# Kernel tuning notes

Measured on AMD Instinct MI355X. Metric: run time of the kernel, lower is better.

## Reference

```python
import jax, jax.numpy as jnp
import numpy as np


def setup_inputs() -> dict:
    key = jax.random.key(0)
    k1, k2, k3 = jax.random.split(key, 3)
    B, Sq, Sk, H, Hk, D = 2, 2048, 2048, 16, 4, 64
    q = jax.random.normal(k1, (B, Sq, H, D), dtype=jnp.float32)
    kv = jax.random.normal(k2, (B, Sk, 2, Hk, D), dtype=jnp.float32)
    key_padding_mask = jax.random.randint(k3, (B, Sk), 0, 2).astype(bool)
    return {"q": q, "kv": kv, "key_padding_mask": key_padding_mask}


def reference(q, kv, key_padding_mask):
    # q: (B, Sq, H, D); kv: (B, Sk, 2, Hk, D); key_padding_mask: (B, Sk) bool (True = keep)
    B, Sq, H, D = q.shape
    Hk = kv.shape[3]
    if Hk != H:
        # GQA: repeat kv heads so (... hkv d) -> (... (hkv g) d)
        kv = jnp.repeat(kv, H // Hk, axis=3)
    k = kv[:, :, 0]  # (B, Sk, H, D)
    v = kv[:, :, 1]  # (B, Sk, H, D)
    softmax_scale = 1.0 / jnp.sqrt(jnp.asarray(D, dtype=q.dtype))
    scores = jnp.einsum('bthd,bshd->bhts', q, k * softmax_scale)  # (B, H, Sq, Sk)
    # additive padding mask: 0 where keep, -10000 where masked (matches torch code)
    pad = jnp.where(key_padding_mask, jnp.asarray(0.0, scores.dtype),
                    jnp.asarray(-10000.0, scores.dtype))
    scores = scores + pad[:, None, None, :]
    attention = jax.nn.softmax(scores, axis=-1)
    # dropout rate is 0.0 -> identity
    output = jnp.einsum('bhts,bshd->bthd', attention, v)  # (B, Sq, H, D)
    return output
```

## Files before the change

kernel.cpp:

```cpp
#include <hip/hip_runtime.h>
#include <hip/hip_bf16.h>
#include <stdint.h>

typedef __bf16 bf16_t;
typedef bf16_t bf16x8 __attribute__((ext_vector_type(8)));
typedef bf16_t bf16x4 __attribute__((ext_vector_type(4)));
typedef float f32x4 __attribute__((ext_vector_type(4)));
typedef float f32x16 __attribute__((ext_vector_type(16)));
typedef uint32_t u32x4 __attribute__((ext_vector_type(4)));
typedef int   i32x4 __attribute__((ext_vector_type(4)));

#define BB 2
#define SQ 2048
#define SK 2048
#define NH 16
#define HKV 4
#define DD 64
#define GQ 4
#define MTILE 128
#define NTILE 64
#define MAXNT 32

#define KTILE_BYTES 8192
#define CNT_OFF   ((size_t)0)
#define CIDX_OFF  ((size_t)1024)
#define PADC_OFF  (CIDX_OFF + (size_t)BB * SK * 4)
#define KC_OFF    ((size_t)65536)
#define VC_OFF    (KC_OFF + (size_t)BB * HKV * MAXNT * KTILE_BYTES)

__device__ __forceinline__ int swzK(int row, int colByte) {
    return row * 128 + (colByte ^ ((row & 7) << 4));
}

#define GLDS(g, l) __builtin_amdgcn_global_load_lds( \
    (const __attribute__((address_space(1))) void*)(g), \
    (__attribute__((address_space(3))) void*)(l), 16, 0, 0)

__global__ __launch_bounds__(256)
void scan_kernel(const int* __restrict__ mask, char* __restrict__ ws)
{
    __shared__ int wtot[4];
    const int b    = blockIdx.x;
    const int tid  = threadIdx.x;
    const int lane = tid & 63;
    const int wid  = tid >> 6;

    int m[8], c = 0;
    {
        const int base = b * SK + tid * 8;
        i32x4 a0 = *(const i32x4*)&mask[base];
        i32x4 a1 = *(const i32x4*)&mask[base + 4];
        #pragma unroll
        for (int j = 0; j < 4; ++j) { m[j] = a0[j] ? 1 : 0; c += m[j]; }
        #pragma unroll
        for (int j = 0; j < 4; ++j) { m[4 + j] = a1[j] ? 1 : 0; c += m[4 + j]; }
    }
    int sc = c;
    #pragma unroll
    for (int off = 1; off < 64; off <<= 1) {
        int n = __shfl_up(sc, off, 64);
        if (lane >= off) sc += n;
    }
    if (lane == 63) wtot[wid] = sc;
    __syncthreads();
    int wbase = 0;
    #pragma unroll
    for (int w = 0; w < 4; ++w) if (w < wid) wbase += wtot[w];
    const int total = wtot[0] + wtot[1] + wtot[2] + wtot[3];

    int* cidx = (int*)(ws + CIDX_OFF) + b * SK;
    int pos = wbase + sc - c;
    #pragma unroll
    for (int j = 0; j < 8; ++j)
        if (m[j]) cidx[pos++] = tid * 8 + j;

    if (tid == 0) ((int*)(ws + CNT_OFF))[b] = total;

    float* padc = (float*)(ws + PADC_OFF) + b * SK;
    for (int i = tid; i < SK; i += 256)
        padc[i] = (i < total) ? 0.f : -30000.f;
}

__global__ __launch_bounds__(256)
void gather_kernel(const float* __restrict__ kv, char* __restrict__ ws)
{
    const int bid  = blockIdx.x;
    const int tile = bid & 31;
    const int bh   = bid >> 5;
    const int hk   = bh & 3;
    const int b    = bh >> 2;

    const int cnt = ((const int*)(ws + CNT_OFF))[b];
    const int nt  = (cnt + 63) >> 6;
    if (tile >= nt) return;

    const int tid = threadIdx.x;
    const int s4  = tid >> 4;
    const int d0  = (tid & 15) * 4;

    const int* cidx = (const int*)(ws + CIDX_OFF) + b * SK;
    bf16_t* Kt = (bf16_t*)(ws + KC_OFF + (size_t)bid * KTILE_BYTES);
    bf16_t* Vt = (bf16_t*)(ws + VC_OFF + (size_t)bid * KTILE_BYTES);

    f32x4 kk4[4], vv4[4];
    #pragma unroll
    for (int p = 0; p < 4; ++p) {
        const int crow = tile * NTILE + s4 * 4 + p;
        if (crow < cnt) {
            const int s = cidx[crow];
            const float* base = kv + (size_t)((b * SK + s) * 2) * (HKV * DD) + hk * DD + d0;
            kk4[p] = *(const f32x4*)base;
            vv4[p] = *(const f32x4*)(base + HKV * DD);
        } else {
            kk4[p] = (f32x4)(0.f);
            vv4[p] = (f32x4)(0.f);
        }
    }
    #pragma unroll
    for (int p = 0; p < 4; ++p) {
        bf16x4 kb;
        #pragma unroll
        for (int j = 0; j < 4; ++j) kb[j] = (bf16_t)kk4[p][j];
        *(bf16x4*)((char*)Kt + swzK(s4 * 4 + p, d0 * 2)) = kb;
    }
    #pragma unroll
    for (int j = 0; j < 4; ++j) {
        bf16x4 tv;
        #pragma unroll
        for (int p = 0; p < 4; ++p) tv[p] = (bf16_t)vv4[p][j];
        *(bf16x4*)((char*)Vt + swzK(d0 + j, s4 * 8)) = tv;
    }
}

__global__ __launch_bounds__(256, 2)
void fattn32p(const float* __restrict__ q, const char* __restrict__ ws,
              float* __restrict__ out)
{
    __shared__ __align__(16) bf16_t Ks[4][NTILE * 64];
    __shared__ __align__(16) bf16_t Vs[4][DD * 64];

    const int tid  = threadIdx.x;
    const int wid  = tid >> 6;
    const int lane = tid & 63;
    const int l31  = lane & 31;
    const int hf   = lane >> 5;
    const int ef   = lane & 7;

    const int bid = (blockIdx.x & 7) * 64 + (blockIdx.x >> 3);
    const int qt  = bid & 15;
    const int bh  = bid >> 4;
    const int hq  = bh & 15;
    const int b   = bh >> 4;
    const int hk  = hq / GQ;

    const int cnt = ((const int*)(ws + CNT_OFF))[b];
    const int nt  = (cnt + 63) >> 6;

    const int qrow0 = qt * MTILE + wid * 32;
    const float SC = 0.18033688011112042f;

    bf16x8 qf[4];
    {
        const float* qp = q + ((size_t)(b * SQ + qrow0 + l31) * NH + hq) * DD;
        #pragma unroll
        for (int kblk = 0; kblk < 4; ++kblk) {
            f32x4 v0 = *(const f32x4*)(qp + kblk * 16 + hf * 8);
            f32x4 v1 = *(const f32x4*)(qp + kblk * 16 + hf * 8 + 4);
            #pragma unroll
            for (int j = 0; j < 4; ++j) {
                qf[kblk][j]     = (bf16_t)(v0[j] * SC);
                qf[kblk][4 + j] = (bf16_t)(v1[j] * SC);
            }
        }
    }

    const char* kgb = ws + KC_OFF + (size_t)((b * HKV + hk) * MAXNT) * KTILE_BYTES;
    const char* vgb = ws + VC_OFF + (size_t)((b * HKV + hk) * MAXNT) * KTILE_BYTES;
    const float* padcb = (const float*)(ws + PADC_OFF) + b * SK;

    auto STAGE = [&](int t, int buf) {
        const char* ksrc = kgb + (size_t)t * KTILE_BYTES + wid * 2048 + lane * 16;
        const char* vsrc = vgb + (size_t)t * KTILE_BYTES + wid * 2048 + lane * 16;
        char* kdst = (char*)Ks[buf] + wid * 2048;
        char* vdst = (char*)Vs[buf] + wid * 2048;
        GLDS(ksrc, kdst);
        GLDS(ksrc + 1024, kdst + 1024);
        GLDS(vsrc, vdst);
        GLDS(vsrc + 1024, vdst + 1024);
    };

    int colX[4];
    #pragma unroll
    for (int kblk = 0; kblk < 4; ++kblk)
        colX[kblk] = (kblk * 32 + hf * 16) ^ (ef << 4);

    f32x16 o0, o1;
    #pragma unroll
    for (int i = 0; i < 16; ++i) { o0[i] = 0.f; o1[i] = 0.f; }
    float l_run = 0.f;

    auto QK = [&](int t, int buf, f32x16& s0, f32x16& s1) {
        if (t == nt - 1) {
            #pragma unroll
            for (int a = 0; a < 4; ++a) {
                f32x4 p0 = *(const f32x4*)(padcb + t * 64 + a * 8 + hf * 4);
                f32x4 p1 = *(const f32x4*)(padcb + t * 64 + 32 + a * 8 + hf * 4);
                #pragma unroll
                for (int c = 0; c < 4; ++c) { s0[a * 4 + c] = p0[c]; s1[a * 4 + c] = p1[c]; }
            }
        } else {
            #pragma unroll
            for (int i = 0; i < 16; ++i) { s0[i] = 0.f; s1[i] = 0.f; }
        }
        __builtin_amdgcn_s_setprio(1);
        #pragma unroll
        for (int kblk = 0; kblk < 4; ++kblk) {
            bf16x8 kf0 = *(const bf16x8*)((char*)Ks[buf] + l31 * 128 + colX[kblk]);
            bf16x8 kf1 = *(const bf16x8*)((char*)Ks[buf] + 4096 + l31 * 128 + colX[kblk]);
            s0 = __builtin_amdgcn_mfma_f32_32x32x16_bf16(kf0, qf[kblk], s0, 0, 0, 0);
            s1 = __builtin_amdgcn_mfma_f32_32x32x16_bf16(kf1, qf[kblk], s1, 0, 0, 0);
        }
        __builtin_amdgcn_s_setprio(0);
    };

    auto SM = [&](f32x16& s0, f32x16& s1, bf16x8* paw) {
        #pragma unroll
        for (int i = 0; i < 16; ++i) {
            s0[i] = __builtin_amdgcn_exp2f(s0[i]);
            s1[i] = __builtin_amdgcn_exp2f(s1[i]);
        }
        float t0 = 0.f, t1 = 0.f, t2 = 0.f, t3 = 0.f;
        #pragma unroll
        for (int i = 0; i < 4; ++i) {
            t0 += s0[i]      + s1[i];
            t1 += s0[4 + i]  + s1[4 + i];
            t2 += s0[8 + i]  + s1[8 + i];
            t3 += s0[12 + i] + s1[12 + i];
        }
        l_run += (t0 + t1) + (t2 + t3);

        #pragma unroll
        for (int ks2 = 0; ks2 < 4; ++ks2) {
            const int aX = (ks2 & 1) * 2;
            uint32_t X0, X1, Y0, Y1;
            #define CVTPK(dst, lo, hi) asm("v_cvt_pk_bf16_f32 %0, %1, %2" : "=v"(dst) : "v"(lo), "v"(hi))
            if (ks2 & 2) {
                CVTPK(X0, s1[4*aX + 0], s1[4*aX + 1]);
                CVTPK(X1, s1[4*aX + 2], s1[4*aX + 3]);
                CVTPK(Y0, s1[4*aX + 4], s1[4*aX + 5]);
                CVTPK(Y1, s1[4*aX + 6], s1[4*aX + 7]);
            } else {
                CVTPK(X0, s0[4*aX + 0], s0[4*aX + 1]);
                CVTPK(X1, s0[4*aX + 2], s0[4*aX + 3]);
                CVTPK(Y0, s0[4*aX + 4], s0[4*aX + 5]);
                CVTPK(Y1, s0[4*aX + 6], s0[4*aX + 7]);
            }
            #undef CVTPK
            asm("v_permlane32_swap_b32 %0, %1" : "+v"(X0), "+v"(Y0));
            asm("v_permlane32_swap_b32 %0, %1" : "+v"(X1), "+v"(Y1));
            union { u32x4 w; bf16x8 v; } u;
            u.w[0] = X0; u.w[1] = X1; u.w[2] = Y0; u.w[3] = Y1;
            paw[ks2] = u.v;
        }
    };

    auto PV = [&](int buf, const bf16x8* paw) {
        __builtin_amdgcn_s_setprio(1);
        #pragma unroll
        for (int ks2 = 0; ks2 < 4; ++ks2) {
            bf16x8 vf0 = *(const bf16x8*)((char*)Vs[buf] + l31 * 128 + colX[ks2]);
            bf16x8 vf1 = *(const bf16x8*)((char*)Vs[buf] + 4096 + l31 * 128 + colX[ks2]);
            o0 = __builtin_amdgcn_mfma_f32_32x32x16_bf16(paw[ks2], vf0, o0, 0, 0, 0);
            o1 = __builtin_amdgcn_mfma_f32_32x32x16_bf16(paw[ks2], vf1, o1, 0, 0, 0);
        }
        __builtin_amdgcn_s_setprio(0);
    };

    STAGE(0, 0);
    if (1 < nt) STAGE(1, 1);

    int t = 0;
    for (; t + 1 < nt; t += 2) {
        const int n2 = (t + 2 < nt) ? 1 : 0;
        const int n3 = (t + 3 < nt) ? 1 : 0;
        if (n2) STAGE(t + 2, (t + 2) & 3);
        if (n3) STAGE(t + 3, (t + 3) & 3);
        if (n2 + n3 == 2)      asm volatile("s_waitcnt vmcnt(8)" ::: "memory");
        else if (n2 + n3 == 1) asm volatile("s_waitcnt vmcnt(4)" ::: "memory");
        else                   asm volatile("s_waitcnt vmcnt(0)" ::: "memory");
        __builtin_amdgcn_s_barrier();
        __builtin_amdgcn_sched_barrier(0);

        f32x16 sA0, sA1, sB0, sB1;
        bf16x8 pawA[4], pawB[4];
        QK(t,     t & 3,       sA0, sA1);
        QK(t + 1, (t + 1) & 3, sB0, sB1);
        SM(sA0, sA1, pawA);
        PV(t & 3, pawA);
        SM(sB0, sB1, pawB);
        PV((t + 1) & 3, pawB);

        __builtin_amdgcn_sched_barrier(0);
        __builtin_amdgcn_s_barrier();
    }
    if (t < nt) {
        asm volatile("s_waitcnt vmcnt(0)" ::: "memory");
        __builtin_amdgcn_s_barrier();
        __builtin_amdgcn_sched_barrier(0);
        f32x16 sA0, sA1;
        bf16x8 pawA[4];
        QK(t, t & 3, sA0, sA1);
        SM(sA0, sA1, pawA);
        PV(t & 3, pawA);
    }

    float lt = l_run + __shfl_xor(l_run, 32, 64);
    #pragma unroll
    for (int r = 0; r < 16; ++r) {
        const int t_r = (r & 3) + 8 * (r >> 2) + 4 * hf;
        const float den = __shfl(lt, t_r, 64);
        const float linv = den > 0.f ? 1.f / den : 0.f;
        float* op = out + ((size_t)(b * SQ + qrow0 + t_r) * NH + hq) * DD + l31;
        op[0]  = o0[r] * linv;
        op[32] = o1[r] * linv;
    }
}

extern "C" void kernel_launch(void* const* d_in, const int* in_sizes, int n_in,
                              void* d_out, int out_size, void* d_ws, size_t ws_size,
                              hipStream_t stream) {
    const float* q    = (const float*)d_in[0];
    const float* kv   = (const float*)d_in[1];
    const int*   mask = (const int*)d_in[2];
    float* out = (float*)d_out;

    scan_kernel<<<BB, 256, 0, stream>>>(mask, (char*)d_ws);
    gather_kernel<<<BB * HKV * MAXNT, 256, 0, stream>>>(kv, (char*)d_ws);
    fattn32p<<<BB * NH * (SQ / MTILE), 256, 0, stream>>>(q, (const char*)d_ws, out);
}
```

Measured before the change: 42.02 us.

## Split KV range across two blocks, fuse scan into gather, add combine pass

Fuses the mask prefix scan into the gather kernel, with each block recomputing the scan and keeping only its 64-entry window in shared memory. The attention kernel is split in two along the key dimension, doubling the grid, cutting LDS to two buffers and raising occupancy to 4 blocks per CU. Unnormalized partial outputs and row sums go to workspace, and a new combine kernel merges and normalizes them. The padding mask is now computed inline instead of loaded, and the LDS swizzle changes to 8-byte granularity with split 64-bit loads. The trade-off is an extra kernel launch plus extra global writes and reads of two full fp32 partial outputs.

```diff
diff --git a/kernel.cpp b/kernel.cpp
--- a/kernel.cpp
+++ b/kernel.cpp
@@ -20,16 +20,19 @@
 #define MTILE 128
 #define NTILE 64
 #define MAXNT 32
+#define NSPLIT 2
 
 #define KTILE_BYTES 8192
 #define CNT_OFF   ((size_t)0)
-#define CIDX_OFF  ((size_t)1024)
-#define PADC_OFF  (CIDX_OFF + (size_t)BB * SK * 4)
-#define KC_OFF    ((size_t)65536)
+#define KC_OFF    ((size_t)4096)
 #define VC_OFF    (KC_OFF + (size_t)BB * HKV * MAXNT * KTILE_BYTES)
-
-__device__ __forceinline__ int swzK(int row, int colByte) {
-    return row * 128 + (colByte ^ ((row & 7) << 4));
+#define OP_OFF    (VC_OFF + (size_t)BB * HKV * MAXNT * KTILE_BYTES)
+#define OP_SPLIT  ((size_t)BB * SQ * NH * DD)
+#define LP_OFF    (OP_OFF + (size_t)NSPLIT * OP_SPLIT * 4)
+#define LP_SPLIT  ((size_t)BB * SQ * NH)
+
+__device__ __forceinline__ int swz8(int row, int colByte) {
+    return row * 128 + (colByte ^ ((row & 15) << 3));
 }
 
 #define GLDS(g, l) __builtin_amdgcn_global_load_lds( \
@@ -37,10 +40,17 @@
     (__attribute__((address_space(3))) void*)(l), 16, 0, 0)
 
 __global__ __launch_bounds__(256)
-void scan_kernel(const int* __restrict__ mask, char* __restrict__ ws)
+void gather_kernel(const float* __restrict__ kv, const int* __restrict__ mask,
+                   char* __restrict__ ws)
 {
     __shared__ int wtot[4];
-    const int b    = blockIdx.x;
+    __shared__ int cwin[NTILE];
+
+    const int bid  = blockIdx.x;
+    const int tile = bid & 31;
+    const int bh   = bid >> 5;
+    const int hk   = bh & 3;
+    const int b    = bh >> 2;
     const int tid  = threadIdx.x;
     const int lane = tid & 63;
     const int wid  = tid >> 6;
@@ -66,48 +76,36 @@
     int wbase = 0;
     #pragma unroll
     for (int w = 0; w < 4; ++w) if (w < wid) wbase += wtot[w];
-    const int total = wtot[0] + wtot[1] + wtot[2] + wtot[3];
-
-    int* cidx = (int*)(ws + CIDX_OFF) + b * SK;
+    const int cnt = wtot[0] + wtot[1] + wtot[2] + wtot[3];
+
+    if (hk == 0 && tile == 0 && tid == 0)
+        ((int*)(ws + CNT_OFF))[b] = cnt;
+
+    const int w0 = tile * NTILE;
     int pos = wbase + sc - c;
     #pragma unroll
     for (int j = 0; j < 8; ++j)
-        if (m[j]) cidx[pos++] = tid * 8 + j;
-
-    if (tid == 0) ((int*)(ws + CNT_OFF))[b] = total;
-
-    float* padc = (float*)(ws + PADC_OFF) + b * SK;
-    for (int i = tid; i < SK; i += 256)
-        padc[i] = (i < total) ? 0.f : -30000.f;
-}
-
-__global__ __launch_bounds__(256)
-void gather_kernel(const float* __restrict__ kv, char* __restrict__ ws)
-{
-    const int bid  = blockIdx.x;
-    const int tile = bid & 31;
-    const int bh   = bid >> 5;
-    const int hk   = bh & 3;
-    const int b    = bh >> 2;
-
-    const int cnt = ((const int*)(ws + CNT_OFF))[b];
-    const int nt  = (cnt + 63) >> 6;
+        if (m[j]) {
+            if (pos >= w0 && pos < w0 + NTILE) cwin[pos - w0] = tid * 8 + j;
+            ++pos;
+        }
+    __syncthreads();
+
+    const int nt = (cnt + 63) >> 6;
     if (tile >= nt) return;
 
-    const int tid = threadIdx.x;
-    const int s4  = tid >> 4;
-    const int d0  = (tid & 15) * 4;
-
-    const int* cidx = (const int*)(ws + CIDX_OFF) + b * SK;
+    const int s4 = tid >> 4;
+    const int d0 = (tid & 15) * 4;
+
     bf16_t* Kt = (bf16_t*)(ws + KC_OFF + (size_t)bid * KTILE_BYTES);
     bf16_t* Vt = (bf16_t*)(ws + VC_OFF + (size_t)bid * KTILE_BYTES);
 
     f32x4 kk4[4], vv4[4];
     #pragma unroll
     for (int p = 0; p < 4; ++p) {
-        const int crow = tile * NTILE + s4 * 4 + p;
+        const int crow = w0 + s4 * 4 + p;
         if (crow < cnt) {
-            const int s = cidx[crow];
+            const int s = cwin[s4 * 4 + p];
             const float* base = kv + (size_t)((b * SK + s) * 2) * (HKV * DD) + hk * DD + d0;
             kk4[p] = *(const f32x4*)base;
             vv4[p] = *(const f32x4*)(base + HKV * DD);
@@ -121,32 +119,32 @@
         bf16x4 kb;
         #pragma unroll
         for (int j = 0; j < 4; ++j) kb[j] = (bf16_t)kk4[p][j];
-        *(bf16x4*)((char*)Kt + swzK(s4 * 4 + p, d0 * 2)) = kb;
+        *(bf16x4*)((char*)Kt + swz8(s4 * 4 + p, d0 * 2)) = kb;
     }
     #pragma unroll
     for (int j = 0; j < 4; ++j) {
         bf16x4 tv;
         #pragma unroll
         for (int p = 0; p < 4; ++p) tv[p] = (bf16_t)vv4[p][j];
-        *(bf16x4*)((char*)Vt + swzK(d0 + j, s4 * 8)) = tv;
-    }
-}
-
-__global__ __launch_bounds__(256, 2)
-void fattn32p(const float* __restrict__ q, const char* __restrict__ ws,
-              float* __restrict__ out)
+        *(bf16x4*)((char*)Vt + swz8(d0 + j, s4 * 8)) = tv;
+    }
+}
+
+__global__ __launch_bounds__(256, 4)
+void fattn_split(const float* __restrict__ q, char* __restrict__ ws)
 {
-    __shared__ __align__(16) bf16_t Ks[4][NTILE * 64];
-    __shared__ __align__(16) bf16_t Vs[4][DD * 64];
+    __shared__ __align__(16) bf16_t Ks[2][NTILE * 64];
+    __shared__ __align__(16) bf16_t Vs[2][DD * 64];
 
     const int tid  = threadIdx.x;
     const int wid  = tid >> 6;
     const int lane = tid & 63;
     const int l31  = lane & 31;
     const int hf   = lane >> 5;
-    const int ef   = lane & 7;
-
-    const int bid = (blockIdx.x & 7) * 64 + (blockIdx.x >> 3);
+
+    const int bidx = (blockIdx.x & 7) * 128 + (blockIdx.x >> 3);
+    const int sp  = bidx & 1;
+    const int bid = bidx >> 1;
     const int qt  = bid & 15;
     const int bh  = bid >> 4;
     const int hq  = bh & 15;
@@ -155,6 +153,9 @@
 
     const int cnt = ((const int*)(ws + CNT_OFF))[b];
     const int nt  = (cnt + 63) >> 6;
+    const int nth = (nt + 1) >> 1;
+    const int tbeg = sp ? nth : 0;
+    const int tend = sp ? nt : nth;
 
     const int qrow0 = qt * MTILE + wid * 32;
     const float SC = 0.18033688011112042f;
@@ -176,7 +177,6 @@
 
     const char* kgb = ws + KC_OFF + (size_t)((b * HKV + hk) * MAXNT) * KTILE_BYTES;
     const char* vgb = ws + VC_OFF + (size_t)((b * HKV + hk) * MAXNT) * KTILE_BYTES;
-    const float* padcb = (const float*)(ws + PADC_OFF) + b * SK;
 
     auto STAGE = [&](int t, int buf) {
         const char* ksrc = kgb + (size_t)t * KTILE_BYTES + wid * 2048 + lane * 16;
@@ -189,41 +189,56 @@
         GLDS(vsrc + 1024, vdst + 1024);
     };
 
-    int colX[4];
-    #pragma unroll
-    for (int kblk = 0; kblk < 4; ++kblk)
-        colX[kblk] = (kblk * 32 + hf * 16) ^ (ef << 4);
+    auto LD8 = [&](const bf16_t* T, int row, int cB) -> bf16x8 {
+        const char* p = (const char*)T + row * 128;
+        const int x = (row & 15) << 3;
+        union { bf16x4 h[2]; bf16x8 v; } u;
+        u.h[0] = *(const bf16x4*)(p + (cB ^ x));
+        u.h[1] = *(const bf16x4*)(p + ((cB + 8) ^ x));
+        return u.v;
+    };
 
     f32x16 o0, o1;
     #pragma unroll
     for (int i = 0; i < 16; ++i) { o0[i] = 0.f; o1[i] = 0.f; }
     float l_run = 0.f;
 
-    auto QK = [&](int t, int buf, f32x16& s0, f32x16& s1) {
+    if (tbeg < tend) STAGE(tbeg, 0);
+
+    for (int t = tbeg; t < tend; ++t) {
+        const int cur = (t - tbeg) & 1;
+        if (t + 1 < tend) {
+            STAGE(t + 1, cur ^ 1);
+            asm volatile("s_waitcnt vmcnt(4)" ::: "memory");
+        } else {
+            asm volatile("s_waitcnt vmcnt(0)" ::: "memory");
+        }
+        __builtin_amdgcn_s_barrier();
+        __builtin_amdgcn_sched_barrier(0);
+
+        f32x16 s0, s1;
         if (t == nt - 1) {
             #pragma unroll
-            for (int a = 0; a < 4; ++a) {
-                f32x4 p0 = *(const f32x4*)(padcb + t * 64 + a * 8 + hf * 4);
-                f32x4 p1 = *(const f32x4*)(padcb + t * 64 + 32 + a * 8 + hf * 4);
-                #pragma unroll
-                for (int c = 0; c < 4; ++c) { s0[a * 4 + c] = p0[c]; s1[a * 4 + c] = p1[c]; }
+            for (int i = 0; i < 16; ++i) {
+                const int sl = (i & 3) + 8 * (i >> 2) + 4 * hf;
+                s0[i] = (t * 64 + sl      < cnt) ? 0.f : -30000.f;
+                s1[i] = (t * 64 + sl + 32 < cnt) ? 0.f : -30000.f;
             }
         } else {
             #pragma unroll
             for (int i = 0; i < 16; ++i) { s0[i] = 0.f; s1[i] = 0.f; }
         }
+
         __builtin_amdgcn_s_setprio(1);
         #pragma unroll
         for (int kblk = 0; kblk < 4; ++kblk) {
-            bf16x8 kf0 = *(const bf16x8*)((char*)Ks[buf] + l31 * 128 + colX[kblk]);
-            bf16x8 kf1 = *(const bf16x8*)((char*)Ks[buf] + 4096 + l31 * 128 + colX[kblk]);
+            bf16x8 kf0 = LD8(Ks[cur], l31,      kblk * 32 + hf * 16);
+            bf16x8 kf1 = LD8(Ks[cur], 32 + l31, kblk * 32 + hf * 16);
             s0 = __builtin_amdgcn_mfma_f32_32x32x16_bf16(kf0, qf[kblk], s0, 0, 0, 0);
             s1 = __builtin_amdgcn_mfma_f32_32x32x16_bf16(kf1, qf[kblk], s1, 0, 0, 0);
         }
         __builtin_amdgcn_s_setprio(0);
-    };
-
-    auto SM = [&](f32x16& s0, f32x16& s1, bf16x8* paw) {
+
         #pragma unroll
         for (int i = 0; i < 16; ++i) {
             s0[i] = __builtin_amdgcn_exp2f(s0[i]);
@@ -239,6 +254,7 @@
         }
         l_run += (t0 + t1) + (t2 + t3);
 
+        bf16x8 paw[4];
         #pragma unroll
         for (int ks2 = 0; ks2 < 4; ++ks2) {
             const int aX = (ks2 & 1) * 2;
@@ -262,68 +278,56 @@
             u.w[0] = X0; u.w[1] = X1; u.w[2] = Y0; u.w[3] = Y1;
             paw[ks2] = u.v;
         }
-    };
-
-    auto PV = [&](int buf, const bf16x8* paw) {
+
         __builtin_amdgcn_s_setprio(1);
         #pragma unroll
         for (int ks2 = 0; ks2 < 4; ++ks2) {
-            bf16x8 vf0 = *(const bf16x8*)((char*)Vs[buf] + l31 * 128 + colX[ks2]);
-            bf16x8 vf1 = *(const bf16x8*)((char*)Vs[buf] + 4096 + l31 * 128 + colX[ks2]);
+            bf16x8 vf0 = LD8(Vs[cur], l31,      ks2 * 32 + hf * 16);
+            bf16x8 vf1 = LD8(Vs[cur], 32 + l31, ks2 * 32 + hf * 16);
             o0 = __builtin_amdgcn_mfma_f32_32x32x16_bf16(paw[ks2], vf0, o0, 0, 0, 0);
             o1 = __builtin_amdgcn_mfma_f32_32x32x16_bf16(paw[ks2], vf1, o1, 0, 0, 0);
         }
         __builtin_amdgcn_s_setprio(0);
-    };
-
-    STAGE(0, 0);
-    if (1 < nt) STAGE(1, 1);
-
-    int t = 0;
-    for (; t + 1 < nt; t += 2) {
-        const int n2 = (t + 2 < nt) ? 1 : 0;
-        const int n3 = (t + 3 < nt) ? 1 : 0;
-        if (n2) STAGE(t + 2, (t + 2) & 3);
-        if (n3) STAGE(t + 3, (t + 3) & 3);
-        if (n2 + n3 == 2)      asm volatile("s_waitcnt vmcnt(8)" ::: "memory");
-        else if (n2 + n3 == 1) asm volatile("s_waitcnt vmcnt(4)" ::: "memory");
-        else                   asm volatile("s_waitcnt vmcnt(0)" ::: "memory");
-        __builtin_amdgcn_s_barrier();
-        __builtin_amdgcn_sched_barrier(0);
-
-        f32x16 sA0, sA1, sB0, sB1;
-        bf16x8 pawA[4], pawB[4];
-        QK(t,     t & 3,       sA0, sA1);
-        QK(t + 1, (t + 1) & 3, sB0, sB1);
-        SM(sA0, sA1, pawA);
-        PV(t & 3, pawA);
-        SM(sB0, sB1, pawB);
-        PV((t + 1) & 3, pawB);
 
         __builtin_amdgcn_sched_barrier(0);
         __builtin_amdgcn_s_barrier();
     }
-    if (t < nt) {
-        asm volatile("s_waitcnt vmcnt(0)" ::: "memory");
-        __builtin_amdgcn_s_barrier();
-        __builtin_amdgcn_sched_barrier(0);
-        f32x16 sA0, sA1;
-        bf16x8 pawA[4];
-        QK(t, t & 3, sA0, sA1);
-        SM(sA0, sA1, pawA);
-        PV(t & 3, pawA);
-    }
 
     float lt = l_run + __shfl_xor(l_run, 32, 64);
+    float* OP = (float*)(ws + OP_OFF) + (size_t)sp * OP_SPLIT;
+    float* LP = (float*)(ws + LP_OFF) + (size_t)sp * LP_SPLIT;
     #pragma unroll
     for (int r = 0; r < 16; ++r) {
         const int t_r = (r & 3) + 8 * (r >> 2) + 4 * hf;
-        const float den = __shfl(lt, t_r, 64);
-        const float linv = den > 0.f ? 1.f / den : 0.f;
-        float* op = out + ((size_t)(b * SQ + qrow0 + t_r) * NH + hq) * DD + l31;
-        op[0]  = o0[r] * linv;
-        op[32] = o1[r] * linv;
-    }
+        const size_t R = ((size_t)(b * SQ + qrow0 + t_r) * NH + hq);
+        OP[R * 64 + l31]      = o0[r];
+        OP[R * 64 + 32 + l31] = o1[r];
+    }
+    if (hf == 0) {
+        const size_t R = ((size_t)(b * SQ + qrow0 + l31) * NH + hq);
+        LP[R] = lt;
+    }
+}
+
+__global__ __launch_bounds__(256)
+void combine_kernel(const char* __restrict__ ws, float* __restrict__ out)
+{
+    const int gid = blockIdx.x * 256 + threadIdx.x;
+    const size_t R = (size_t)(gid >> 4);
+    const int c4 = (gid & 15) * 4;
+    const float* P0 = (const float*)(ws + OP_OFF);
+    const float* P1 = P0 + OP_SPLIT;
+    const float* L0 = (const float*)(ws + LP_OFF);
+    const float* L1 = L0 + LP_SPLIT;
+
+    f32x4 a = *(const f32x4*)&P0[R * 64 + c4];
+    f32x4 c = *(const f32x4*)&P1[R * 64 + c4];
+    const float den = L0[R] + L1[R];
+    const float inv = den > 0.f ? 1.f / den : 0.f;
+    f32x4 o;
+    #pragma unroll
+    for (int j = 0; j < 4; ++j) o[j] = (a[j] + c[j]) * inv;
+    *(f32x4*)&out[R * 64 + c4] = o;
 }
 
 extern "C" void kernel_launch(void* const* d_in, const int* in_sizes, int n_in,
@@ -334,7 +338,7 @@
     const int*   mask = (const int*)d_in[2];
     float* out = (float*)d_out;
 
-    scan_kernel<<<BB, 256, 0, stream>>>(mask, (char*)d_ws);
-    gather_kernel<<<BB * HKV * MAXNT, 256, 0, stream>>>(kv, (char*)d_ws);
-    fattn32p<<<BB * NH * (SQ / MTILE), 256, 0, stream>>>(q, (const char*)d_ws, out);
-}
+    gather_kernel<<<BB * HKV * MAXNT, 256, 0, stream>>>(kv, mask, (char*)d_ws);
+    fattn_split<<<BB * NH * (SQ / MTILE) * NSPLIT, 256, 0, stream>>>(q, (char*)d_ws);
+    combine_kernel<<<(BB * SQ * NH * 16) / 256, 256, 0, stream>>>((const char*)d_ws, out);
+}
```

Result: slower. 51.11 us (+21.6%).

## Fuse mask scan into gather kernel and compute padding inline

Applied to the files above, without the earlier changes.

Merges the scan and gather kernels so each gather block redoes the prefix scan over the mask and keeps only its own 64-entry index window in shared memory, which drops one launch and the global index buffer. The padding bias is now computed in registers from the count rather than read from a workspace array. The K/V swizzle moves to an 8-byte granularity over 16 rows, so each 16-byte fragment read becomes two 8-byte LDS reads. The cost is the scan being repeated across 256 blocks and twice as many LDS read instructions in the inner loop.

```diff
diff --git a/kernel.cpp b/kernel.cpp
--- a/kernel.cpp
+++ b/kernel.cpp
@@ -23,13 +23,11 @@
 
 #define KTILE_BYTES 8192
 #define CNT_OFF   ((size_t)0)
-#define CIDX_OFF  ((size_t)1024)
-#define PADC_OFF  (CIDX_OFF + (size_t)BB * SK * 4)
-#define KC_OFF    ((size_t)65536)
+#define KC_OFF    ((size_t)4096)
 #define VC_OFF    (KC_OFF + (size_t)BB * HKV * MAXNT * KTILE_BYTES)
 
-__device__ __forceinline__ int swzK(int row, int colByte) {
-    return row * 128 + (colByte ^ ((row & 7) << 4));
+__device__ __forceinline__ int swz8(int row, int colByte) {
+    return row * 128 + (colByte ^ ((row & 15) << 3));
 }
 
 #define GLDS(g, l) __builtin_amdgcn_global_load_lds( \
@@ -37,10 +35,17 @@
     (__attribute__((address_space(3))) void*)(l), 16, 0, 0)
 
 __global__ __launch_bounds__(256)
-void scan_kernel(const int* __restrict__ mask, char* __restrict__ ws)
+void gather_kernel(const float* __restrict__ kv, const int* __restrict__ mask,
+                   char* __restrict__ ws)
 {
     __shared__ int wtot[4];
-    const int b    = blockIdx.x;
+    __shared__ int cwin[NTILE];
+
+    const int bid  = blockIdx.x;
+    const int tile = bid & 31;
+    const int bh   = bid >> 5;
+    const int hk   = bh & 3;
+    const int b    = bh >> 2;
     const int tid  = threadIdx.x;
     const int lane = tid & 63;
     const int wid  = tid >> 6;
@@ -66,48 +71,36 @@
     int wbase = 0;
     #pragma unroll
     for (int w = 0; w < 4; ++w) if (w < wid) wbase += wtot[w];
-    const int total = wtot[0] + wtot[1] + wtot[2] + wtot[3];
-
-    int* cidx = (int*)(ws + CIDX_OFF) + b * SK;
+    const int cnt = wtot[0] + wtot[1] + wtot[2] + wtot[3];
+
+    if (hk == 0 && tile == 0 && tid == 0)
+        ((int*)(ws + CNT_OFF))[b] = cnt;
+
+    const int w0 = tile * NTILE;
     int pos = wbase + sc - c;
     #pragma unroll
     for (int j = 0; j < 8; ++j)
-        if (m[j]) cidx[pos++] = tid * 8 + j;
-
-    if (tid == 0) ((int*)(ws + CNT_OFF))[b] = total;
-
-    float* padc = (float*)(ws + PADC_OFF) + b * SK;
-    for (int i = tid; i < SK; i += 256)
-        padc[i] = (i < total) ? 0.f : -30000.f;
-}
-
-__global__ __launch_bounds__(256)
-void gather_kernel(const float* __restrict__ kv, char* __restrict__ ws)
-{
-    const int bid  = blockIdx.x;
-    const int tile = bid & 31;
-    const int bh   = bid >> 5;
-    const int hk   = bh & 3;
-    const int b    = bh >> 2;
-
-    const int cnt = ((const int*)(ws + CNT_OFF))[b];
-    const int nt  = (cnt + 63) >> 6;
+        if (m[j]) {
+            if (pos >= w0 && pos < w0 + NTILE) cwin[pos - w0] = tid * 8 + j;
+            ++pos;
+        }
+    __syncthreads();
+
+    const int nt = (cnt + 63) >> 6;
     if (tile >= nt) return;
 
-    const int tid = threadIdx.x;
-    const int s4  = tid >> 4;
-    const int d0  = (tid & 15) * 4;
-
-    const int* cidx = (const int*)(ws + CIDX_OFF) + b * SK;
+    const int s4 = tid >> 4;
+    const int d0 = (tid & 15) * 4;
+
     bf16_t* Kt = (bf16_t*)(ws + KC_OFF + (size_t)bid * KTILE_BYTES);
     bf16_t* Vt = (bf16_t*)(ws + VC_OFF + (size_t)bid * KTILE_BYTES);
 
     f32x4 kk4[4], vv4[4];
     #pragma unroll
     for (int p = 0; p < 4; ++p) {
-        const int crow = tile * NTILE + s4 * 4 + p;
+        const int crow = w0 + s4 * 4 + p;
         if (crow < cnt) {
-            const int s = cidx[crow];
+            const int s = cwin[s4 * 4 + p];
             const float* base = kv + (size_t)((b * SK + s) * 2) * (HKV * DD) + hk * DD + d0;
             kk4[p] = *(const f32x4*)base;
             vv4[p] = *(const f32x4*)(base + HKV * DD);
@@ -121,14 +114,14 @@
         bf16x4 kb;
         #pragma unroll
         for (int j = 0; j < 4; ++j) kb[j] = (bf16_t)kk4[p][j];
-        *(bf16x4*)((char*)Kt + swzK(s4 * 4 + p, d0 * 2)) = kb;
+        *(bf16x4*)((char*)Kt + swz8(s4 * 4 + p, d0 * 2)) = kb;
     }
     #pragma unroll
     for (int j = 0; j < 4; ++j) {
         bf16x4 tv;
         #pragma unroll
         for (int p = 0; p < 4; ++p) tv[p] = (bf16_t)vv4[p][j];
-        *(bf16x4*)((char*)Vt + swzK(d0 + j, s4 * 8)) = tv;
+        *(bf16x4*)((char*)Vt + swz8(d0 + j, s4 * 8)) = tv;
     }
 }
 
@@ -144,7 +137,6 @@
     const int lane = tid & 63;
     const int l31  = lane & 31;
     const int hf   = lane >> 5;
-    const int ef   = lane & 7;
 
     const int bid = (blockIdx.x & 7) * 64 + (blockIdx.x >> 3);
     const int qt  = bid & 15;
@@ -176,7 +168,6 @@
 
     const char* kgb = ws + KC_OFF + (size_t)((b * HKV + hk) * MAXNT) * KTILE_BYTES;
     const char* vgb = ws + VC_OFF + (size_t)((b * HKV + hk) * MAXNT) * KTILE_BYTES;
-    const float* padcb = (const float*)(ws + PADC_OFF) + b * SK;
 
     auto STAGE = [&](int t, int buf) {
         const char* ksrc = kgb + (size_t)t * KTILE_BYTES + wid * 2048 + lane * 16;
@@ -189,10 +180,14 @@
         GLDS(vsrc + 1024, vdst + 1024);
     };
 
-    int colX[4];
-    #pragma unroll
-    for (int kblk = 0; kblk < 4; ++kblk)
-        colX[kblk] = (kblk * 32 + hf * 16) ^ (ef << 4);
+    auto LD8 = [&](const bf16_t* T, int row, int cB) -> bf16x8 {
+        const char* p = (const char*)T + row * 128;
+        const int x = (row & 15) << 3;
+        union { bf16x4 h[2]; bf16x8 v; } u;
+        u.h[0] = *(const bf16x4*)(p + (cB ^ x));
+        u.h[1] = *(const bf16x4*)(p + ((cB + 8) ^ x));
+        return u.v;
+    };
 
     f32x16 o0, o1;
     #pragma unroll
@@ -202,11 +197,10 @@
     auto QK = [&](int t, int buf, f32x16& s0, f32x16& s1) {
         if (t == nt - 1) {
             #pragma unroll
-            for (int a = 0; a < 4; ++a) {
-                f32x4 p0 = *(const f32x4*)(padcb + t * 64 + a * 8 + hf * 4);
-                f32x4 p1 = *(const f32x4*)(padcb + t * 64 + 32 + a * 8 + hf * 4);
-                #pragma unroll
-                for (int c = 0; c < 4; ++c) { s0[a * 4 + c] = p0[c]; s1[a * 4 + c] = p1[c]; }
+            for (int i = 0; i < 16; ++i) {
+                const int sl = (i & 3) + 8 * (i >> 2) + 4 * hf;
+                s0[i] = (t * 64 + sl      < cnt) ? 0.f : -30000.f;
+                s1[i] = (t * 64 + sl + 32 < cnt) ? 0.f : -30000.f;
             }
         } else {
             #pragma unroll
@@ -215,8 +209,8 @@
         __builtin_amdgcn_s_setprio(1);
         #pragma unroll
         for (int kblk = 0; kblk < 4; ++kblk) {
-            bf16x8 kf0 = *(const bf16x8*)((char*)Ks[buf] + l31 * 128 + colX[kblk]);
-            bf16x8 kf1 = *(const bf16x8*)((char*)Ks[buf] + 4096 + l31 * 128 + colX[kblk]);
+            bf16x8 kf0 = LD8(Ks[buf], l31,      kblk * 32 + hf * 16);
+            bf16x8 kf1 = LD8(Ks[buf], 32 + l31, kblk * 32 + hf * 16);
             s0 = __builtin_amdgcn_mfma_f32_32x32x16_bf16(kf0, qf[kblk], s0, 0, 0, 0);
             s1 = __builtin_amdgcn_mfma_f32_32x32x16_bf16(kf1, qf[kblk], s1, 0, 0, 0);
         }
@@ -268,8 +262,8 @@
         __builtin_amdgcn_s_setprio(1);
         #pragma unroll
         for (int ks2 = 0; ks2 < 4; ++ks2) {
-            bf16x8 vf0 = *(const bf16x8*)((char*)Vs[buf] + l31 * 128 + colX[ks2]);
-            bf16x8 vf1 = *(const bf16x8*)((char*)Vs[buf] + 4096 + l31 * 128 + colX[ks2]);
+            bf16x8 vf0 = LD8(Vs[buf], l31,      ks2 * 32 + hf * 16);
+            bf16x8 vf1 = LD8(Vs[buf], 32 + l31, ks2 * 32 + hf * 16);
             o0 = __builtin_amdgcn_mfma_f32_32x32x16_bf16(paw[ks2], vf0, o0, 0, 0, 0);
             o1 = __builtin_amdgcn_mfma_f32_32x32x16_bf16(paw[ks2], vf1, o1, 0, 0, 0);
         }
@@ -334,7 +328,6 @@
     const int*   mask = (const int*)d_in[2];
     float* out = (float*)d_out;
 
-    scan_kernel<<<BB, 256, 0, stream>>>(mask, (char*)d_ws);
-    gather_kernel<<<BB * HKV * MAXNT, 256, 0, stream>>>(kv, (char*)d_ws);
+    gather_kernel<<<BB * HKV * MAXNT, 256, 0, stream>>>(kv, mask, (char*)d_ws);
     fattn32p<<<BB * NH * (SQ / MTILE), 256, 0, stream>>>(q, (const char*)d_ws, out);
 }
```

Result: faster. 39.85 us, median of 2 (-5.2%).
